# Kernel tuning notes

Hardware: AMD Instinct MI355X
Metric: run time of the kernel (lower is better)

The kernel has to match this reference:

```python
import jax, jax.numpy as jnp
import numpy as np

B, S, D, H = 2, 2048, 1024, 16
DK = D // H


def setup_inputs() -> dict:
    key = jax.random.key(0)
    ks = jax.random.split(key, 12)
    sc = 1.0 / np.sqrt(D)
    inp = {
        "q": jax.random.normal(ks[0], (B, S, D), jnp.float32),
        "k": jax.random.normal(ks[1], (B, S, D), jnp.float32),
        "v": jax.random.normal(ks[2], (B, S, D), jnp.float32),
        # causal mask, broadcastable over batch and heads
        "mask": jnp.tril(jnp.ones((S, S), jnp.int32))[None, None],
        "Wq": jax.random.normal(ks[3], (D, D), jnp.float32) * sc,
        "bq": jax.random.normal(ks[4], (D,), jnp.float32) * 0.02,
        "Wk": jax.random.normal(ks[5], (D, D), jnp.float32) * sc,
        "bk": jax.random.normal(ks[6], (D,), jnp.float32) * 0.02,
        "Wv": jax.random.normal(ks[7], (D, D), jnp.float32) * sc,
        "bv": jax.random.normal(ks[8], (D,), jnp.float32) * 0.02,
        "Wo": jax.random.normal(ks[9], (D, D), jnp.float32) * sc,
        "bo": jax.random.normal(ks[10], (D,), jnp.float32) * 0.02,
    }
    return inp


def reference(q, k, v, mask, Wq, bq, Wk, bk, Wv, bv, Wo, bo):
    b, s, _ = q.shape
    # QKV projections (torch Linear: x @ W.T + b)
    qh = (q @ Wq.T + bq).reshape(b, s, H, DK).transpose(0, 2, 1, 3)  # [B,H,S,DK]
    kh = (k @ Wk.T + bk).reshape(b, -1, H, DK).transpose(0, 2, 1, 3)
    vh = (v @ Wv.T + bv).reshape(b, -1, H, DK).transpose(0, 2, 1, 3)
    scores = jnp.einsum("bhqd,bhkd->bhqk", qh, kh) / np.sqrt(DK)  # [B,H,S,S]
    scores = jnp.where(mask == 0, jnp.float32(-1e9), scores)
    attn = jax.nn.softmax(scores, axis=-1)
    # dropout p=0.0 (eval) -> identity
    x = jnp.einsum("bhqk,bhkd->bhqd", attn, vh)  # [B,H,S,DK]
    x = x.transpose(0, 2, 1, 3).reshape(b, s, H * DK)
    return x @ Wo.T + bo
```

## Files before the change

kernel.cpp:

```cpp
#include <hip/hip_runtime.h>
#include <hip/hip_bf16.h>
#include <cstdint>
#include <cstddef>

using u16   = unsigned short;
using u32   = uint32_t;
using u16x4 = __attribute__((ext_vector_type(4))) unsigned short;
using u16x8 = __attribute__((ext_vector_type(8))) unsigned short;
using s16x8 = __attribute__((ext_vector_type(8))) short;
using f32x4 = __attribute__((ext_vector_type(4))) float;
using f32x16 = __attribute__((ext_vector_type(16))) float;

#define B_DIM  2
#define S_DIM  2048
#define D_DIM  1024
#define H_DIM  16
#define DK_DIM 64

__device__ __forceinline__ u16 f2bf(float f) {
  union { float f; uint32_t u; } c; c.f = f;
  uint32_t u = c.u;
  return (u16)((u + 0x7FFFu + ((u >> 16) & 1u)) >> 16);
}
__device__ __forceinline__ float bf2f(u16 v) {
  union { uint32_t u; float f; } c; c.u = (uint32_t)v << 16;
  return c.f;
}

__device__ __forceinline__ void gload16(const void* g, void* l) {
  __builtin_amdgcn_global_load_lds(
      (const __attribute__((address_space(1))) void*)g,
      (__attribute__((address_space(3))) void*)l, 16, 0, 0);
}

__device__ __forceinline__ int chunk_base(int qt) {
  return (qt < 4) ? qt
       : (qt < 8) ? 4 + 2 * (qt - 4)
       : (qt < 12) ? 12 + 3 * (qt - 8)
       : 24 + 4 * (qt - 12);
}

__global__ __launch_bounds__(256) void cast_bf16_kernel(
    const float* s0, const float* s1, const float* s2, const float* s3,
    u16* d0, u16* d1, u16* d2, u16* d3, int n)
{
  const float* s; u16* d;
  switch (blockIdx.y) {
    case 0: s = s0; d = d0; break;
    case 1: s = s1; d = d1; break;
    case 2: s = s2; d = d2; break;
    default: s = s3; d = d3; break;
  }
  int i = (blockIdx.x * 256 + threadIdx.x) * 8;
  if (i >= n) return;
  f32x4 a = *(const f32x4*)(s + i);
  f32x4 b = *(const f32x4*)(s + i + 4);
  u16x8 ov;
  ov[0] = f2bf(a[0]); ov[1] = f2bf(a[1]); ov[2] = f2bf(a[2]); ov[3] = f2bf(a[3]);
  ov[4] = f2bf(b[0]); ov[5] = f2bf(b[1]); ov[6] = f2bf(b[2]); ov[7] = f2bf(b[3]);
  *(u16x8*)(d + i) = ov;
}

#define BM 128
#define BN 64
#define BK 64

__device__ __forceinline__ void gemm_bt_core(
    const u16* __restrict__ A, const u16* __restrict__ W,
    const float* __restrict__ bias, void* __restrict__ out, int mode,
    int mtile, int ntile, float oscale)
{
  __shared__ u16 Alds[BM * BK];
  __shared__ u16 Blds[BN * BK];
  const int K = 1024;
  const int tid = threadIdx.x;
  const int w = tid >> 6, l = tid & 63;
  const int lr = l & 15, lg = l >> 4;
  const int wr = w >> 1, wc = w & 1;
  const int m0 = mtile * BM, n0 = ntile * BN;

  f32x4 acc[4][2] = {};

  for (int kt = 0; kt < K / BK; ++kt) {
    const int k0 = kt * BK;
    #pragma unroll
    for (int i = 0; i < 4; ++i) {
      int c = i * 256 + tid;
      int r = c >> 3;
      int cb = ((c & 7) << 4) ^ ((r & 7) << 4);
      gload16((const char*)(A + (size_t)(m0 + r) * K + k0) + cb,
              (char*)Alds + i * 4096 + w * 1024);
    }
    #pragma unroll
    for (int i = 0; i < 2; ++i) {
      int c = i * 256 + tid;
      int r = c >> 3;
      int cb = ((c & 7) << 4) ^ ((r & 7) << 4);
      gload16((const char*)(W + (size_t)(n0 + r) * K + k0) + cb,
              (char*)Blds + i * 4096 + w * 1024);
    }
    __syncthreads();
    #pragma unroll
    for (int ks = 0; ks < 2; ++ks) {
      s16x8 af[4], bf[2];
      #pragma unroll
      for (int mi = 0; mi < 4; ++mi) {
        int r = wr * 64 + mi * 16 + lr;
        int kb = (ks * 64 + lg * 16) ^ ((r & 7) << 4);
        af[mi] = *(const s16x8*)((const char*)Alds + r * 128 + kb);
      }
      #pragma unroll
      for (int ni = 0; ni < 2; ++ni) {
        int r = wc * 32 + ni * 16 + lr;
        int kb = (ks * 64 + lg * 16) ^ ((r & 7) << 4);
        bf[ni] = *(const s16x8*)((const char*)Blds + r * 128 + kb);
      }
      #pragma unroll
      for (int mi = 0; mi < 4; ++mi)
        #pragma unroll
        for (int ni = 0; ni < 2; ++ni)
          acc[mi][ni] = __builtin_amdgcn_mfma_f32_16x16x32_bf16(
              af[mi], bf[ni], acc[mi][ni], 0, 0, 0);
    }
    __syncthreads();
  }

  const int mbase = m0 + wr * 64 + lg * 4;
  const int nbase = n0 + wc * 32 + lr;
  #pragma unroll
  for (int ni = 0; ni < 2; ++ni) {
    int n = nbase + ni * 16;
    float bb = bias[n];
    #pragma unroll
    for (int mi = 0; mi < 4; ++mi) {
      int mr = mbase + mi * 16;
      f32x4 vv = acc[mi][ni];
      if (mode == 2) {
        float* o = (float*)out;
        #pragma unroll
        for (int r = 0; r < 4; ++r) o[(size_t)(mr + r) * 1024 + n] = vv[r] + bb;
      } else if (mode == 0) {
        u16* o = (u16*)out;
        #pragma unroll
        for (int r = 0; r < 4; ++r)
          o[(size_t)(mr + r) * 1024 + n] = f2bf((vv[r] + bb) * oscale);
      } else if (mode == 3) {
        u16* o = (u16*)out;
        int h = n >> 6, d = n & 63;
        int db = d >> 4, hi8 = (d >> 3) & 1, e = d & 7;
        int bb_ = mr >> 11, j = mr & (S_DIM - 1);
        int jt = j >> 6, rh = (j >> 5) & 1, lq0 = j & 31;
        size_t base = (((size_t)(bb_ * H_DIM + h) * 32 + jt) * 8 + (db * 2 + rh))
                      * 512 + (size_t)(hi8 * 32) * 8 + e;
        #pragma unroll
        for (int r = 0; r < 4; ++r)
          o[base + (size_t)(lq0 + r) * 8] = f2bf(vv[r] + bb);
      } else {
        u16* o = (u16*)out;
        int h = n >> 6, dk = n & 63;
        int rh = dk >> 5, lq = dk & 31;
        int bb_ = mr >> 11, j = mr & (S_DIM - 1);
        int jt = j >> 6, jj = j & 63;
        int db = jj >> 4, hi8 = (jj >> 3) & 1, e0 = jj & 7;
        size_t base = (((size_t)(bb_ * H_DIM + h) * 32 + jt) * 8 + (db * 2 + rh))
                      * 512 + (size_t)(hi8 * 32 + lq) * 8 + e0;
        u16x4 pk;
        #pragma unroll
        for (int r = 0; r < 4; ++r) pk[r] = f2bf(vv[r] + bb);
        *(u16x4*)(o + base) = pk;
      }
    }
  }
}

__global__ __launch_bounds__(256, 5) void qkv_gemm_kernel(
    const u16* xq, const u16* xk, const u16* xv,
    const u16* wq, const u16* wk, const u16* wv,
    const float* bq, const float* bk, const float* bv,
    u16* qlin, u16* kfragb, u16* vfragb)
{
  const int f = blockIdx.x;
  const int xcd = f & 7;
  const int s = f >> 3;
  const int z = s >> 6;
  const int r = s & 63;
  const int mtile = xcd * 4 + (r >> 4);
  const int ntile = r & 15;

  const u16* A = (z == 0) ? xq : (z == 1) ? xk : xv;
  const u16* W = (z == 0) ? wq : (z == 1) ? wk : wv;
  const float* bias = (z == 0) ? bq : (z == 1) ? bk : bv;
  void* out = (z == 0) ? (void*)qlin : (z == 1) ? (void*)kfragb : (void*)vfragb;
  gemm_bt_core(A, W, bias, out, (z == 0) ? 0 : (z == 1) ? 3 : 1, mtile, ntile,
               (z == 0) ? 0.125f * 1.44269504f : 1.0f);
}

__global__ __launch_bounds__(256, 5) void oproj_kernel(
    const u16* aout, const u16* wo, const float* bo, float* out)
{
  const int f = blockIdx.x;
  const int xcd = f & 7;
  const int s = f >> 3;
  const int mtile = xcd * 4 + (s >> 4);
  const int ntile = s & 15;
  gemm_bt_core(aout, wo, bo, (void*)out, 2, mtile, ntile, 1.0f);
}

__global__ __launch_bounds__(256, 2) void attn_kernel(
    const u16* __restrict__ qlin, const u16* __restrict__ kfrag,
    const u16* __restrict__ vfrag, u16* __restrict__ opart,
    float* __restrict__ lpart)
{
  const int tid = threadIdx.x;
  const int w = tid >> 6, l = tid & 63;
  const int lq = l & 31, hi = l >> 5;

  const int f = blockIdx.x;
  const int bh = f & 31;
  const int g = f >> 5;
  int qt, ch;
  if (g < 16)      { qt = 15 - (g >> 2);        ch = g & 3; }
  else if (g < 28) { qt = 11 - (g - 16) / 3;    ch = (g - 16) % 3; }
  else if (g < 36) { qt = 7 - ((g - 28) >> 1);  ch = (g - 28) & 1; }
  else             { qt = 3 - (g - 36);         ch = 0; }
  const int T  = 2 * qt + 2;
  const int nc = (T + 7) >> 3;
  const int jlo = (ch * T) / nc;
  const int jhi = ((ch + 1) * T) / nc;
  const int b = bh >> 4, h = bh & 15;

  const int qb  = qt * 128 + w * 32;
  const int myq = qb + lq;
  const int jtend_w = (qb + 31) >> 6;
  const int jend = (jhi < jtend_w + 1) ? jhi : (jtend_w + 1);

  s16x8 qf[4];
  {
    const u16* qptr = qlin + (size_t)(b * S_DIM + myq) * D_DIM + h * DK_DIM + hi * 8;
    #pragma unroll
    for (int db = 0; db < 4; ++db) qf[db] = *(const s16x8*)(qptr + db * 16);
  }

  f32x16 o0 = {}, o1 = {};
  float l_run = 0.f;

  const u16* kbase = kfrag + (size_t)bh * 32 * 4096;
  const u16* vbase = vfrag + (size_t)bh * 32 * 4096;

  s16x8 kf2[8], vf2[8];
  #pragma unroll
  for (int fk = 0; fk < 8; ++fk)
    kf2[fk] = *(const s16x8*)(kbase + (size_t)jlo * 4096 + fk * 512 + (size_t)l * 8);
  #pragma unroll
  for (int fk = 0; fk < 8; ++fk)
    vf2[fk] = *(const s16x8*)(vbase + (size_t)jlo * 4096 + fk * 512 + (size_t)l * 8);

  #pragma unroll 1
  for (int jt = jlo; jt < jend; ++jt) {
    const int j0 = jt * 64;

    f32x16 s0 = {}, s1 = {};
    #pragma unroll
    for (int db = 0; db < 4; ++db) {
      s0 = __builtin_amdgcn_mfma_f32_32x32x16_bf16(kf2[db * 2 + 0], qf[db], s0, 0, 0, 0);
      s1 = __builtin_amdgcn_mfma_f32_32x32x16_bf16(kf2[db * 2 + 1], qf[db], s1, 0, 0, 0);
    }

    if (jt + 1 < jend) {
      const u16* kbn = kbase + (size_t)(jt + 1) * 4096;
      #pragma unroll
      for (int fk = 0; fk < 8; ++fk)
        kf2[fk] = *(const s16x8*)(kbn + fk * 512 + (size_t)l * 8);
    }

    if (j0 + 63 > qb) {
      #pragma unroll
      for (int r = 0; r < 16; ++r) {
        int kr = (r & 3) + 8 * (r >> 2) + 4 * hi;
        if (j0 + kr > myq)      s0[r] = -1e30f;
        if (j0 + 32 + kr > myq) s1[r] = -1e30f;
      }
    }

    u32 wds[16];
    float ls = 0.f;
    #pragma unroll
    for (int i = 0; i < 8; ++i) {
      float pa = __builtin_amdgcn_exp2f(s0[2 * i]);
      float pb = __builtin_amdgcn_exp2f(s0[2 * i + 1]);
      ls += pa + pb;
      wds[i] = (u32)f2bf(pa) | ((u32)f2bf(pb) << 16);
      float pc = __builtin_amdgcn_exp2f(s1[2 * i]);
      float pd = __builtin_amdgcn_exp2f(s1[2 * i + 1]);
      ls += pc + pd;
      wds[8 + i] = (u32)f2bf(pc) | ((u32)f2bf(pd) << 16);
    }
    l_run += ls;

    #pragma unroll
    for (int ks = 0; ks < 4; ++ks) {
      u32 w0 = wds[4 * ks], w1 = wds[4 * ks + 1];
      u32 w2 = wds[4 * ks + 2], w3 = wds[4 * ks + 3];
      u32 ta = __shfl_xor(hi ? w0 : w2, 32);
      u32 tb = __shfl_xor(hi ? w1 : w3, 32);
      union { u32 u[4]; s16x8 v; } pf;
      pf.u[0] = hi ? ta : w0;
      pf.u[1] = hi ? tb : w1;
      pf.u[2] = hi ? w2 : ta;
      pf.u[3] = hi ? w3 : tb;
      o0 = __builtin_amdgcn_mfma_f32_32x32x16_bf16(vf2[ks * 2 + 0], pf.v, o0, 0, 0, 0);
      o1 = __builtin_amdgcn_mfma_f32_32x32x16_bf16(vf2[ks * 2 + 1], pf.v, o1, 0, 0, 0);
    }

    if (jt + 1 < jend) {
      const u16* vbn = vbase + (size_t)(jt + 1) * 4096;
      #pragma unroll
      for (int fk = 0; fk < 8; ++fk)
        vf2[fk] = *(const s16x8*)(vbn + fk * 512 + (size_t)l * 8);
    }
  }

  const size_t gslot = (size_t)bh * 40 + chunk_base(qt) + ch;
  u16* ob = opart + ((gslot * 128) + w * 32 + lq) * 64;
  #pragma unroll
  for (int rq = 0; rq < 4; ++rq) {
    u16x4 pk0, pk1;
    #pragma unroll
    for (int j = 0; j < 4; ++j) {
      pk0[j] = f2bf(o0[rq * 4 + j]);
      pk1[j] = f2bf(o1[rq * 4 + j]);
    }
    *(u16x4*)(ob + rq * 8 + hi * 4)      = pk0;
    *(u16x4*)(ob + 32 + rq * 8 + hi * 4) = pk1;
  }
  float lt = l_run + __shfl_xor(l_run, 32);
  if (hi == 0) lpart[gslot * 128 + w * 32 + lq] = lt;
}

__global__ __launch_bounds__(256) void attn_combine_kernel(
    const u16* __restrict__ opart, const float* __restrict__ lpart,
    u16* __restrict__ aout)
{
  const int f = blockIdx.x;
  const int bh = f & 31, qt = f >> 5;
  const int b = bh >> 4, h = bh & 15;
  const int nc = (2 * qt + 9) >> 3;
  const int cs = chunk_base(qt);

  const int t = threadIdx.x;
  const int row = t >> 1, dbase = (t & 1) * 32;
  float acc[32] = {};
  float lsum = 0.f;
  for (int c = 0; c < nc; ++c) {
    const size_t slot = (size_t)bh * 40 + cs + c;
    const u16* pr = opart + ((slot * 128) + row) * 64 + dbase;
    #pragma unroll
    for (int v4 = 0; v4 < 4; ++v4) {
      u16x8 vv = *(const u16x8*)(pr + v4 * 8);
      #pragma unroll
      for (int j = 0; j < 8; ++j) acc[v4 * 8 + j] += bf2f(vv[j]);
    }
    lsum += lpart[slot * 128 + row];
  }
  float inv = 1.f / lsum;
  u16* orow = aout + ((size_t)b * S_DIM + qt * 128 + row) * D_DIM + h * 64 + dbase;
  #pragma unroll
  for (int v4 = 0; v4 < 4; ++v4) {
    u16x8 ov;
    #pragma unroll
    for (int j = 0; j < 8; ++j) ov[j] = f2bf(acc[v4 * 8 + j] * inv);
    *(u16x8*)(orow + v4 * 8) = ov;
  }
}

extern "C" void kernel_launch(void* const* d_in, const int* in_sizes, int n_in,
                              void* d_out, int out_size, void* d_ws, size_t ws_size,
                              hipStream_t stream)
{
  (void)in_sizes; (void)n_in; (void)out_size; (void)ws_size;
  const float* q  = (const float*)d_in[0];
  const float* k  = (const float*)d_in[1];
  const float* v  = (const float*)d_in[2];
  const float* Wq = (const float*)d_in[4];
  const float* bq = (const float*)d_in[5];
  const float* Wk = (const float*)d_in[6];
  const float* bk = (const float*)d_in[7];
  const float* Wv = (const float*)d_in[8];
  const float* bv = (const float*)d_in[9];
  const float* Wo = (const float*)d_in[10];
  const float* bo = (const float*)d_in[11];
  float* out = (float*)d_out;

  const size_t XSZ = (size_t)B_DIM * S_DIM * D_DIM;
  const size_t WSZ = (size_t)D_DIM * D_DIM;

  u16* p = (u16*)d_ws;
  u16* qbf  = p; p += XSZ;
  u16* kbf  = p; p += XSZ;
  u16* vbf  = p; p += XSZ;
  u16* wqb  = p; p += WSZ;
  u16* wkb  = p; p += WSZ;
  u16* wvb  = p; p += WSZ;
  u16* wob  = p; p += WSZ;
  u16* qlin   = p; p += XSZ;
  u16* kfragb = p; p += XSZ;
  u16* vfragb = p; p += XSZ;
  u16* aoutb  = p; p += XSZ;

  u16*   opart = (u16*)d_ws;
  float* lpart = (float*)((char*)d_ws + (size_t)1280 * 128 * 64 * 2);

  cast_bf16_kernel<<<dim3((unsigned)(XSZ / 8 / 256), 3), 256, 0, stream>>>(
      q, k, v, nullptr, qbf, kbf, vbf, nullptr, (int)XSZ);
  cast_bf16_kernel<<<dim3((unsigned)(WSZ / 8 / 256), 4), 256, 0, stream>>>(
      Wq, Wk, Wv, Wo, wqb, wkb, wvb, wob, (int)WSZ);
  qkv_gemm_kernel<<<1536, 256, 0, stream>>>(
      qbf, kbf, vbf, wqb, wkb, wvb, bq, bk, bv, qlin, kfragb, vfragb);
  attn_kernel<<<1280, 256, 0, stream>>>(qlin, kfragb, vfragb, opart, lpart);
  attn_combine_kernel<<<512, 256, 0, stream>>>(opart, lpart, aoutb);
  oproj_kernel<<<512, 256, 0, stream>>>(aoutb, wob, bo, out);
}
```

Before: 123.1 us.

## Make each attention wave own a 64-row query tile sharing loaded K/V

Each wave now processes two 32-row query halves (64 rows total) against the same K/V fragments, so every K/V load feeds twice as many MFMAs and the causal mask only runs on the diagonal tile. Work is re-partitioned per wave into 64-row query slots with chunking over key tiles, halving the attention grid and doubling the combine grid with 64-row partial outputs. The cost is more registers per wave (two Q fragment sets and four output accumulators), which can reduce occupancy, and less block-level parallelism.

```diff
diff --git a/kernel.cpp b/kernel.cpp
--- a/kernel.cpp
+++ b/kernel.cpp
@@ -33,11 +33,11 @@
       (__attribute__((address_space(3))) void*)l, 16, 0, 0);
 }
 
-__device__ __forceinline__ int chunk_base(int qt) {
-  return (qt < 4) ? qt
-       : (qt < 8) ? 4 + 2 * (qt - 4)
-       : (qt < 12) ? 12 + 3 * (qt - 8)
-       : 24 + 4 * (qt - 12);
+__device__ __forceinline__ int chunk_base64(int qw) {
+  return (qw < 8)  ? qw
+       : (qw < 16) ? 8  + 2 * (qw - 8)
+       : (qw < 24) ? 24 + 3 * (qw - 16)
+       :             48 + 4 * (qw - 24);
 }
 
 __global__ __launch_bounds__(256) void cast_bf16_kernel(
@@ -218,31 +218,35 @@
   const int f = blockIdx.x;
   const int bh = f & 31;
   const int g = f >> 5;
-  int qt, ch;
-  if (g < 16)      { qt = 15 - (g >> 2);        ch = g & 3; }
-  else if (g < 28) { qt = 11 - (g - 16) / 3;    ch = (g - 16) % 3; }
-  else if (g < 36) { qt = 7 - ((g - 28) >> 1);  ch = (g - 28) & 1; }
-  else             { qt = 3 - (g - 36);         ch = 0; }
-  const int T  = 2 * qt + 2;
-  const int nc = (T + 7) >> 3;
+  const int slot = (19 - g) * 4 + w;
+  int qw, ch;
+  if (slot < 8)       { qw = slot;                    ch = 0; }
+  else if (slot < 24) { qw = 8 + ((slot - 8) >> 1);   ch = (slot - 8) & 1; }
+  else if (slot < 48) { qw = 16 + (slot - 24) / 3;    ch = (slot - 24) % 3; }
+  else                { qw = 24 + ((slot - 48) >> 2); ch = (slot - 48) & 3; }
+  const int T  = qw + 1;
+  const int nc = (qw + 8) >> 3;
   const int jlo = (ch * T) / nc;
   const int jhi = ((ch + 1) * T) / nc;
   const int b = bh >> 4, h = bh & 15;
 
-  const int qb  = qt * 128 + w * 32;
-  const int myq = qb + lq;
-  const int jtend_w = (qb + 31) >> 6;
-  const int jend = (jhi < jtend_w + 1) ? jhi : (jtend_w + 1);
-
-  s16x8 qf[4];
+  const int qb   = qw * 64;
+  const int myqA = qb + lq;
+  const int myqB = qb + 32 + lq;
+
+  s16x8 qfA[4], qfB[4];
   {
-    const u16* qptr = qlin + (size_t)(b * S_DIM + myq) * D_DIM + h * DK_DIM + hi * 8;
-    #pragma unroll
-    for (int db = 0; db < 4; ++db) qf[db] = *(const s16x8*)(qptr + db * 16);
-  }
-
-  f32x16 o0 = {}, o1 = {};
-  float l_run = 0.f;
+    const u16* qpA = qlin + (size_t)(b * S_DIM + myqA) * D_DIM + h * DK_DIM + hi * 8;
+    const u16* qpB = qlin + (size_t)(b * S_DIM + myqB) * D_DIM + h * DK_DIM + hi * 8;
+    #pragma unroll
+    for (int db = 0; db < 4; ++db) {
+      qfA[db] = *(const s16x8*)(qpA + db * 16);
+      qfB[db] = *(const s16x8*)(qpB + db * 16);
+    }
+  }
+
+  f32x16 oA0 = {}, oA1 = {}, oB0 = {}, oB1 = {};
+  float lA = 0.f, lB = 0.f;
 
   const u16* kbase = kfrag + (size_t)bh * 32 * 4096;
   const u16* vbase = vfrag + (size_t)bh * 32 * 4096;
@@ -256,51 +260,58 @@
     vf2[fk] = *(const s16x8*)(vbase + (size_t)jlo * 4096 + fk * 512 + (size_t)l * 8);
 
   #pragma unroll 1
-  for (int jt = jlo; jt < jend; ++jt) {
+  for (int jt = jlo; jt < jhi; ++jt) {
     const int j0 = jt * 64;
+    const bool diag = (jt == qw);
 
     f32x16 s0 = {}, s1 = {};
     #pragma unroll
     for (int db = 0; db < 4; ++db) {
-      s0 = __builtin_amdgcn_mfma_f32_32x32x16_bf16(kf2[db * 2 + 0], qf[db], s0, 0, 0, 0);
-      s1 = __builtin_amdgcn_mfma_f32_32x32x16_bf16(kf2[db * 2 + 1], qf[db], s1, 0, 0, 0);
-    }
-
-    if (jt + 1 < jend) {
+      s0 = __builtin_amdgcn_mfma_f32_32x32x16_bf16(kf2[db * 2 + 0], qfA[db], s0, 0, 0, 0);
+      s1 = __builtin_amdgcn_mfma_f32_32x32x16_bf16(kf2[db * 2 + 1], qfA[db], s1, 0, 0, 0);
+    }
+    if (diag) {
+      #pragma unroll
+      for (int r = 0; r < 16; ++r) {
+        int kr = (r & 3) + 8 * (r >> 2) + 4 * hi;
+        if (j0 + kr > myqA)      s0[r] = -1e30f;
+        if (j0 + 32 + kr > myqA) s1[r] = -1e30f;
+      }
+    }
+    u32 wdsA[16];
+    {
+      float ls = 0.f;
+      #pragma unroll
+      for (int i = 0; i < 8; ++i) {
+        float pa = __builtin_amdgcn_exp2f(s0[2 * i]);
+        float pb = __builtin_amdgcn_exp2f(s0[2 * i + 1]);
+        ls += pa + pb;
+        wdsA[i] = (u32)f2bf(pa) | ((u32)f2bf(pb) << 16);
+        float pc = __builtin_amdgcn_exp2f(s1[2 * i]);
+        float pd = __builtin_amdgcn_exp2f(s1[2 * i + 1]);
+        ls += pc + pd;
+        wdsA[8 + i] = (u32)f2bf(pc) | ((u32)f2bf(pd) << 16);
+      }
+      lA += ls;
+    }
+
+    f32x16 t0 = {}, t1 = {};
+    #pragma unroll
+    for (int db = 0; db < 4; ++db) {
+      t0 = __builtin_amdgcn_mfma_f32_32x32x16_bf16(kf2[db * 2 + 0], qfB[db], t0, 0, 0, 0);
+      t1 = __builtin_amdgcn_mfma_f32_32x32x16_bf16(kf2[db * 2 + 1], qfB[db], t1, 0, 0, 0);
+    }
+    if (jt + 1 < jhi) {
       const u16* kbn = kbase + (size_t)(jt + 1) * 4096;
       #pragma unroll
       for (int fk = 0; fk < 8; ++fk)
         kf2[fk] = *(const s16x8*)(kbn + fk * 512 + (size_t)l * 8);
     }
 
-    if (j0 + 63 > qb) {
-      #pragma unroll
-      for (int r = 0; r < 16; ++r) {
-        int kr = (r & 3) + 8 * (r >> 2) + 4 * hi;
-        if (j0 + kr > myq)      s0[r] = -1e30f;
-        if (j0 + 32 + kr > myq) s1[r] = -1e30f;
-      }
-    }
-
-    u32 wds[16];
-    float ls = 0.f;
-    #pragma unroll
-    for (int i = 0; i < 8; ++i) {
-      float pa = __builtin_amdgcn_exp2f(s0[2 * i]);
-      float pb = __builtin_amdgcn_exp2f(s0[2 * i + 1]);
-      ls += pa + pb;
-      wds[i] = (u32)f2bf(pa) | ((u32)f2bf(pb) << 16);
-      float pc = __builtin_amdgcn_exp2f(s1[2 * i]);
-      float pd = __builtin_amdgcn_exp2f(s1[2 * i + 1]);
-      ls += pc + pd;
-      wds[8 + i] = (u32)f2bf(pc) | ((u32)f2bf(pd) << 16);
-    }
-    l_run += ls;
-
     #pragma unroll
     for (int ks = 0; ks < 4; ++ks) {
-      u32 w0 = wds[4 * ks], w1 = wds[4 * ks + 1];
-      u32 w2 = wds[4 * ks + 2], w3 = wds[4 * ks + 3];
+      u32 w0 = wdsA[4 * ks], w1 = wdsA[4 * ks + 1];
+      u32 w2 = wdsA[4 * ks + 2], w3 = wdsA[4 * ks + 3];
       u32 ta = __shfl_xor(hi ? w0 : w2, 32);
       u32 tb = __shfl_xor(hi ? w1 : w3, 32);
       union { u32 u[4]; s16x8 v; } pf;
@@ -308,11 +319,50 @@
       pf.u[1] = hi ? tb : w1;
       pf.u[2] = hi ? w2 : ta;
       pf.u[3] = hi ? w3 : tb;
-      o0 = __builtin_amdgcn_mfma_f32_32x32x16_bf16(vf2[ks * 2 + 0], pf.v, o0, 0, 0, 0);
-      o1 = __builtin_amdgcn_mfma_f32_32x32x16_bf16(vf2[ks * 2 + 1], pf.v, o1, 0, 0, 0);
-    }
-
-    if (jt + 1 < jend) {
+      oA0 = __builtin_amdgcn_mfma_f32_32x32x16_bf16(vf2[ks * 2 + 0], pf.v, oA0, 0, 0, 0);
+      oA1 = __builtin_amdgcn_mfma_f32_32x32x16_bf16(vf2[ks * 2 + 1], pf.v, oA1, 0, 0, 0);
+    }
+
+    if (diag) {
+      #pragma unroll
+      for (int r = 0; r < 16; ++r) {
+        int kr = (r & 3) + 8 * (r >> 2) + 4 * hi;
+        if (j0 + kr > myqB)      t0[r] = -1e30f;
+        if (j0 + 32 + kr > myqB) t1[r] = -1e30f;
+      }
+    }
+    u32 wdsB[16];
+    {
+      float ls = 0.f;
+      #pragma unroll
+      for (int i = 0; i < 8; ++i) {
+        float pa = __builtin_amdgcn_exp2f(t0[2 * i]);
+        float pb = __builtin_amdgcn_exp2f(t0[2 * i + 1]);
+        ls += pa + pb;
+        wdsB[i] = (u32)f2bf(pa) | ((u32)f2bf(pb) << 16);
+        float pc = __builtin_amdgcn_exp2f(t1[2 * i]);
+        float pd = __builtin_amdgcn_exp2f(t1[2 * i + 1]);
+        ls += pc + pd;
+        wdsB[8 + i] = (u32)f2bf(pc) | ((u32)f2bf(pd) << 16);
+      }
+      lB += ls;
+    }
+
+    #pragma unroll
+    for (int ks = 0; ks < 4; ++ks) {
+      u32 w0 = wdsB[4 * ks], w1 = wdsB[4 * ks + 1];
+      u32 w2 = wdsB[4 * ks + 2], w3 = wdsB[4 * ks + 3];
+      u32 ta = __shfl_xor(hi ? w0 : w2, 32);
+      u32 tb = __shfl_xor(hi ? w1 : w3, 32);
+      union { u32 u[4]; s16x8 v; } pf;
+      pf.u[0] = hi ? ta : w0;
+      pf.u[1] = hi ? tb : w1;
+      pf.u[2] = hi ? w2 : ta;
+      pf.u[3] = hi ? w3 : tb;
+      oB0 = __builtin_amdgcn_mfma_f32_32x32x16_bf16(vf2[ks * 2 + 0], pf.v, oB0, 0, 0, 0);
+      oB1 = __builtin_amdgcn_mfma_f32_32x32x16_bf16(vf2[ks * 2 + 1], pf.v, oB1, 0, 0, 0);
+    }
+    if (jt + 1 < jhi) {
       const u16* vbn = vbase + (size_t)(jt + 1) * 4096;
       #pragma unroll
       for (int fk = 0; fk < 8; ++fk)
@@ -320,21 +370,30 @@
     }
   }
 
-  const size_t gslot = (size_t)bh * 40 + chunk_base(qt) + ch;
-  u16* ob = opart + ((gslot * 128) + w * 32 + lq) * 64;
+  const size_t gslot = (size_t)bh * 80 + chunk_base64(qw) + ch;
+  u16* obA = opart + ((gslot * 64) + lq) * 64;
+  u16* obB = opart + ((gslot * 64) + 32 + lq) * 64;
   #pragma unroll
   for (int rq = 0; rq < 4; ++rq) {
-    u16x4 pk0, pk1;
+    u16x4 a0, a1, b0, b1;
     #pragma unroll
     for (int j = 0; j < 4; ++j) {
-      pk0[j] = f2bf(o0[rq * 4 + j]);
-      pk1[j] = f2bf(o1[rq * 4 + j]);
-    }
-    *(u16x4*)(ob + rq * 8 + hi * 4)      = pk0;
-    *(u16x4*)(ob + 32 + rq * 8 + hi * 4) = pk1;
-  }
-  float lt = l_run + __shfl_xor(l_run, 32);
-  if (hi == 0) lpart[gslot * 128 + w * 32 + lq] = lt;
+      a0[j] = f2bf(oA0[rq * 4 + j]);
+      a1[j] = f2bf(oA1[rq * 4 + j]);
+      b0[j] = f2bf(oB0[rq * 4 + j]);
+      b1[j] = f2bf(oB1[rq * 4 + j]);
+    }
+    *(u16x4*)(obA + rq * 8 + hi * 4)      = a0;
+    *(u16x4*)(obA + 32 + rq * 8 + hi * 4) = a1;
+    *(u16x4*)(obB + rq * 8 + hi * 4)      = b0;
+    *(u16x4*)(obB + 32 + rq * 8 + hi * 4) = b1;
+  }
+  float ltA = lA + __shfl_xor(lA, 32);
+  float ltB = lB + __shfl_xor(lB, 32);
+  if (hi == 0) {
+    lpart[gslot * 64 + lq]      = ltA;
+    lpart[gslot * 64 + 32 + lq] = ltB;
+  }
 }
 
 __global__ __launch_bounds__(256) void attn_combine_kernel(
@@ -342,30 +401,30 @@
     u16* __restrict__ aout)
 {
   const int f = blockIdx.x;
-  const int bh = f & 31, qt = f >> 5;
+  const int bh = f & 31, qw = f >> 5;
   const int b = bh >> 4, h = bh & 15;
-  const int nc = (2 * qt + 9) >> 3;
-  const int cs = chunk_base(qt);
+  const int nc = (qw + 8) >> 3;
+  const int cs = chunk_base64(qw);
 
   const int t = threadIdx.x;
-  const int row = t >> 1, dbase = (t & 1) * 32;
-  float acc[32] = {};
+  const int row = t >> 2, dbase = (t & 3) * 16;
+  float acc[16] = {};
   float lsum = 0.f;
   for (int c = 0; c < nc; ++c) {
-    const size_t slot = (size_t)bh * 40 + cs + c;
-    const u16* pr = opart + ((slot * 128) + row) * 64 + dbase;
-    #pragma unroll
-    for (int v4 = 0; v4 < 4; ++v4) {
+    const size_t slot = (size_t)bh * 80 + cs + c;
+    const u16* pr = opart + ((slot * 64) + row) * 64 + dbase;
+    #pragma unroll
+    for (int v4 = 0; v4 < 2; ++v4) {
       u16x8 vv = *(const u16x8*)(pr + v4 * 8);
       #pragma unroll
       for (int j = 0; j < 8; ++j) acc[v4 * 8 + j] += bf2f(vv[j]);
     }
-    lsum += lpart[slot * 128 + row];
+    lsum += lpart[slot * 64 + row];
   }
   float inv = 1.f / lsum;
-  u16* orow = aout + ((size_t)b * S_DIM + qt * 128 + row) * D_DIM + h * 64 + dbase;
+  u16* orow = aout + ((size_t)b * S_DIM + qw * 64 + row) * D_DIM + h * 64 + dbase;
   #pragma unroll
-  for (int v4 = 0; v4 < 4; ++v4) {
+  for (int v4 = 0; v4 < 2; ++v4) {
     u16x8 ov;
     #pragma unroll
     for (int j = 0; j < 8; ++j) ov[j] = f2bf(acc[v4 * 8 + j] * inv);
@@ -408,7 +467,7 @@
   u16* aoutb  = p; p += XSZ;
 
   u16*   opart = (u16*)d_ws;
-  float* lpart = (float*)((char*)d_ws + (size_t)1280 * 128 * 64 * 2);
+  float* lpart = (float*)((char*)d_ws + (size_t)2560 * 64 * 64 * 2);
 
   cast_bf16_kernel<<<dim3((unsigned)(XSZ / 8 / 256), 3), 256, 0, stream>>>(
       q, k, v, nullptr, qbf, kbf, vbf, nullptr, (int)XSZ);
@@ -416,7 +475,7 @@
       Wq, Wk, Wv, Wo, wqb, wkb, wvb, wob, (int)WSZ);
   qkv_gemm_kernel<<<1536, 256, 0, stream>>>(
       qbf, kbf, vbf, wqb, wkb, wvb, bq, bk, bv, qlin, kfragb, vfragb);
-  attn_kernel<<<1280, 256, 0, stream>>>(qlin, kfragb, vfragb, opart, lpart);
-  attn_combine_kernel<<<512, 256, 0, stream>>>(opart, lpart, aoutb);
+  attn_kernel<<<640, 256, 0, stream>>>(qlin, kfragb, vfragb, opart, lpart);
+  attn_combine_kernel<<<1024, 256, 0, stream>>>(opart, lpart, aoutb);
   oproj_kernel<<<512, 256, 0, stream>>>(aoutb, wob, bo, out);
 }
```

Result: slower. 139.0 us (+12.9%).
